# Kernel optimization log

Hardware: AMD Instinct MI355X
Metric: run time of the kernel (lower is better)

The kernel has to match this reference:

```python
import jax, jax.numpy as jnp
import numpy as np

COMMITMENT_COST = 0.25
ENTROPY_WEIGHT = 0.1
EPS = 1e-10


def setup_inputs() -> dict:
    key = jax.random.key(0)
    k1, k2 = jax.random.split(key)
    B, L, D, K = 8, 4096, 256, 4096
    z = jax.random.normal(k1, (B, L, D), dtype=jnp.float32)
    # torch init: uniform(-1/K, 1/K)
    codebook_weight = jax.random.uniform(k2, (K, D), dtype=jnp.float32,
                                         minval=-1.0 / K, maxval=1.0 / K)
    return {"z": z, "codebook_weight": codebook_weight}


def reference(z, codebook_weight):
    B, L, D = z.shape
    z_flat = z.reshape(-1, D)                       # [N, D]
    # squared euclidean distances: [N, K]
    d2 = (jnp.sum(z_flat ** 2, axis=1, keepdims=True)
          + jnp.sum(codebook_weight ** 2, axis=1)
          - 2.0 * z_flat @ codebook_weight.T)
    indices = jnp.argmin(d2, axis=1)                # [N]
    z_q_flat = codebook_weight[indices]             # gather [N, D]
    z_q = z_q_flat.reshape(B, L, D)

    codebook_loss = jnp.mean((z_q - jax.lax.stop_gradient(z)) ** 2)
    commitment_loss = jnp.mean((jax.lax.stop_gradient(z_q) - z) ** 2)

    probs = jax.nn.softmax(-d2, axis=1)             # [N, K]
    avg_probs = probs.mean(axis=0)                  # [K]
    entropy = -jnp.sum(avg_probs * jnp.log(avg_probs + EPS))
    entropy_loss = -entropy

    codebook_commitment_loss = codebook_loss + COMMITMENT_COST * commitment_loss
    scaled_entropy_loss = ENTROPY_WEIGHT * entropy_loss
    vq_loss = codebook_commitment_loss + scaled_entropy_loss

    # straight-through estimator
    z_q_ste = z + jax.lax.stop_gradient(z_q - z)
    indices_out = indices.reshape(B, L)
    return (z_q_ste, indices_out, vq_loss, codebook_commitment_loss, scaled_entropy_loss)
```

## Files before the change

kernel.cpp:

```cpp
#include <hip/hip_runtime.h>
#include <stdint.h>

#define NROWS 32768
#define KC 4096
#define DIM 256
#define BM 32
#define NCT 128
#define TPW 32
#define CAP 40
#define KAPPA 0.99960f
#define K2L2E 2.88539008f
#define L2E 1.44269504f

#define OUT_IDX (NROWS * DIM)
#define OUT_SCAL (OUT_IDX + NROWS)

#define WS_CNORM 0
#define WS_ZNORM 16384
#define WS_LOSS  147456
#define WS_AVGP8 147712
#define WS_FRAG  278784

typedef __bf16 bf8 __attribute__((ext_vector_type(8)));
typedef float f16v __attribute__((ext_vector_type(16)));

__device__ __forceinline__ unsigned ford(float f) {
  unsigned u = __float_as_uint(f);
  return (u & 0x80000000u) ? ~u : (u | 0x80000000u);
}

__device__ __forceinline__ float np_rownorm256(const float* __restrict__ p) {
  float h[2];
  #pragma unroll
  for (int half = 0; half < 2; ++half) {
    const float* b = p + half * 128;
    float r[8];
    #pragma unroll
    for (int j = 0; j < 8; ++j) { float v = b[j]; r[j] = __fmul_rn(v, v); }
    for (int i = 8; i < 128; i += 8) {
      #pragma unroll
      for (int j = 0; j < 8; ++j) {
        float v = b[i + j];
        r[j] = __fadd_rn(r[j], __fmul_rn(v, v));
      }
    }
    h[half] = __fadd_rn(
        __fadd_rn(__fadd_rn(r[0], r[1]), __fadd_rn(r[2], r[3])),
        __fadd_rn(__fadd_rn(r[4], r[5]), __fadd_rn(r[6], r[7])));
  }
  return __fadd_rn(h[0], h[1]);
}

__global__ void k_norms(const float* __restrict__ cbw, const float* __restrict__ z,
                        float* __restrict__ cnorm, float* __restrict__ znorm) {
  int r = blockIdx.x * 256 + threadIdx.x;
  if (r < KC) cnorm[r] = np_rownorm256(cbw + (size_t)r * DIM);
  else {
    int q = r - KC;
    if (q < NROWS) znorm[q] = np_rownorm256(z + (size_t)q * DIM);
  }
}

__global__ void k_frag(const float* __restrict__ cbw, __bf16* __restrict__ frag) {
  int idx = blockIdx.x * 256 + threadIdx.x;
  int c = idx >> 5, u = idx & 31;
  int ds = u >> 1, half = u & 1;
  int ct = c >> 5, m = c & 31;
  int lane = half * 32 + m;
  const float* src = cbw + (size_t)c * DIM + ds * 16 + half * 8;
  float4 a = *(const float4*)src;
  float4 b = *(const float4*)(src + 4);
  bf8 h;
  h[0] = (__bf16)a.x; h[1] = (__bf16)a.y; h[2] = (__bf16)a.z; h[3] = (__bf16)a.w;
  h[4] = (__bf16)b.x; h[5] = (__bf16)b.y; h[6] = (__bf16)b.z; h[7] = (__bf16)b.w;
  *(bf8*)(frag + ((size_t)(ct * 16 + ds) * 64 + lane) * 8) = h;
}

__device__ __forceinline__ float exact_d2(const float* __restrict__ zr,
                                          const float* __restrict__ cr,
                                          float rn, float cn) {
  float mm = 0.f;
  for (int d = 0; d < DIM; d += 4) {
    float4 zv = *(const float4*)(zr + d);
    float4 cv = *(const float4*)(cr + d);
    mm = __builtin_fmaf(zv.x, cv.x, mm);
    mm = __builtin_fmaf(zv.y, cv.y, mm);
    mm = __builtin_fmaf(zv.z, cv.z, mm);
    mm = __builtin_fmaf(zv.w, cv.w, mm);
  }
  return __fsub_rn(__fadd_rn(rn, cn), __fmul_rn(2.f, mm));
}

__device__ __forceinline__ void tile_mfma(const __bf16* __restrict__ Aimg,
                                          const __bf16* __restrict__ tb,
                                          int lane, f16v& acc) {
  #pragma unroll
  for (int r = 0; r < 16; ++r) acc[r] = 0.f;
  #pragma unroll
  for (int ds = 0; ds < 16; ++ds) {
    bf8 Bf = *(const bf8*)(tb + (ds * 64 + lane) * 8);
    bf8 Af = *(const bf8*)&Aimg[((size_t)ds * 64 + lane) * 8];
    acc = __builtin_amdgcn_mfma_f32_32x32x16_bf16(Af, Bf, acc, 0, 0, 0);
  }
}

__global__ __launch_bounds__(256, 4) void k_main(
    const float* __restrict__ z, const float* __restrict__ cbw,
    const float* __restrict__ cnorm, const float* __restrict__ znorm,
    const __bf16* __restrict__ frag, float* __restrict__ out,
    float* __restrict__ avgp8, double* __restrict__ losssum) {
  __shared__ __bf16 Aimg[16 * 64 * 8];
  union CP { int cand[BM][CAP]; float pcol[KC]; };
  __shared__ CP cp;
  __shared__ int ccount[BM];
  __shared__ unsigned rowmaxU[BM];
  __shared__ unsigned long long rowkey[BM];
  __shared__ float esumL[BM], invR[BM], lred[256];
  __shared__ int idxr[BM];

  const int t = threadIdx.x;
  const int lane = t & 63, wv = t >> 6;
  const int ln31 = lane & 31, lh = lane >> 5;
  const int row0 = blockIdx.x * BM;

  if (t < BM) {
    ccount[t] = 0; rowmaxU[t] = 0u; rowkey[t] = ~0ULL; esumL[t] = 0.f;
  }

  #pragma unroll
  for (int i = 0; i < 4; ++i) {
    int idx = t * 4 + i;
    int l = idx & 63, ds = idx >> 6;
    int row = l & 31, d0 = ds * 16 + (l >> 5) * 8;
    const float* src = z + (size_t)(row0 + row) * DIM + d0;
    float4 a = *(const float4*)src;
    float4 b = *(const float4*)(src + 4);
    bf8 h;
    h[0] = (__bf16)a.x; h[1] = (__bf16)a.y; h[2] = (__bf16)a.z; h[3] = (__bf16)a.w;
    h[4] = (__bf16)b.x; h[5] = (__bf16)b.y; h[6] = (__bf16)b.z; h[7] = (__bf16)b.w;
    *(bf8*)&Aimg[((size_t)ds * 64 + l) * 8] = h;
  }
  __syncthreads();

  {
    const int ct = wv * TPW;
    f16v acc;
    tile_mfma(Aimg, frag + (size_t)ct * 8192, lane, acc);
    const float cnl = cnorm[ct * 32 + ln31] * L2E;
    #pragma unroll
    for (int r = 0; r < 16; ++r) {
      const int row = (r & 3) + 8 * (r >> 2) + 4 * lh;
      float e = exp2f(__builtin_fmaf(acc[r], K2L2E, -cnl));
      atomicMax(&rowmaxU[row], __float_as_uint(e));
    }
  }
  __syncthreads();

  float es[16], em[16];
  #pragma unroll
  for (int i = 0; i < 16; ++i) { es[i] = 0.f; em[i] = 0.f; }

  for (int ti = 0; ti < TPW; ++ti) {
    const int ct = wv * TPW + ti;
    f16v acc;
    tile_mfma(Aimg, frag + (size_t)ct * 8192, lane, acc);
    const float cnl = cnorm[ct * 32 + ln31] * L2E;
    #pragma unroll
    for (int r = 0; r < 16; ++r) {
      const int row = (r & 3) + 8 * (r >> 2) + 4 * lh;
      float e = exp2f(__builtin_fmaf(acc[r], K2L2E, -cnl));
      es[r] += e;
      float rm = fmaxf(em[r], __uint_as_float(rowmaxU[row]));
      if (e > rm) { atomicMax(&rowmaxU[row], __float_as_uint(e)); rm = e; }
      em[r] = rm;
      if (e >= rm * KAPPA) {
        int slot = atomicAdd(&ccount[row], 1);
        if (slot < CAP) cp.cand[row][slot] = ct * 32 + ln31;
      }
    }
  }

  #pragma unroll
  for (int r = 0; r < 16; ++r) {
    float e = es[r];
    #pragma unroll
    for (int off = 16; off > 0; off >>= 1) e += __shfl_xor(e, off);
    if (ln31 == 0) {
      const int row = (r & 3) + 8 * (r >> 2) + 4 * lh;
      atomicAdd(&esumL[row], e);
    }
  }
  __syncthreads();
  if (t < BM) invR[t] = 1.0f / esumL[t];
  __syncthreads();

  {
    int r = t & 31, q = t >> 5;
    int cnt = ccount[r];
    const float* zr = z + (size_t)(row0 + r) * DIM;
    float rn = znorm[row0 + r];
    if (cnt <= CAP) {
      for (int s = q; s < cnt; s += 8) {
        int k = cp.cand[r][s];
        float d2 = exact_d2(zr, cbw + (size_t)k * DIM, rn, cnorm[k]);
        atomicMin(&rowkey[r], (((unsigned long long)ford(d2)) << 32) | (unsigned)k);
      }
    } else {
      for (int k = q; k < KC; k += 8) {
        float d2 = exact_d2(zr, cbw + (size_t)k * DIM, rn, cnorm[k]);
        atomicMin(&rowkey[r], (((unsigned long long)ford(d2)) << 32) | (unsigned)k);
      }
    }
  }
  __syncthreads();
  if (t < BM) {
    int idx = (int)(rowkey[t] & 0xFFFFFFFFULL);
    idxr[t] = idx;
    out[OUT_IDX + row0 + t] = (float)idx;
  }
  __syncthreads();

  float lacc = 0.f;
  for (int r = 0; r < BM; ++r) {
    int idx = idxr[r];
    float zq = cbw[(size_t)idx * DIM + t];
    float zv = z[(size_t)(row0 + r) * DIM + t];
    float df = __fsub_rn(zq, zv);
    out[(size_t)(row0 + r) * DIM + t] = __fadd_rn(zv, df);
    lacc += df * df;
  }
  lred[t] = lacc;
  __syncthreads();
  #pragma unroll
  for (int s = 128; s > 0; s >>= 1) {
    if (t < s) lred[t] += lred[t + s];
    __syncthreads();
  }
  if (t == 0) atomicAdd(losssum, (double)lred[0]);

  float ir[16];
  #pragma unroll
  for (int r = 0; r < 16; ++r)
    ir[r] = invR[(r & 3) + 8 * (r >> 2) + 4 * lh];
  __syncthreads();

  for (int ti = 0; ti < TPW; ++ti) {
    const int ct = wv * TPW + ti;
    f16v acc;
    tile_mfma(Aimg, frag + (size_t)ct * 8192, lane, acc);
    const float cnl = cnorm[ct * 32 + ln31] * L2E;
    float s = 0.f;
    #pragma unroll
    for (int r = 0; r < 16; ++r) {
      float e = exp2f(__builtin_fmaf(acc[r], K2L2E, -cnl));
      s = __builtin_fmaf(e, ir[r], s);
    }
    s += __shfl_xor(s, 32);
    if (lh == 0) cp.pcol[ct * 32 + ln31] = s;
  }
  __syncthreads();
  {
    float* shadow = avgp8 + (size_t)(blockIdx.x & 7) * KC;
    #pragma unroll
    for (int i = 0; i < 16; ++i)
      atomicAdd(&shadow[t + 256 * i], cp.pcol[t + 256 * i]);
  }
}

__global__ void k_final(const float* __restrict__ avgp8,
                        const double* __restrict__ losssum,
                        float* __restrict__ out) {
  const int t = threadIdx.x;
  double part = 0.0;
  for (int k = t; k < KC; k += 256) {
    float a4 = 0.f;
    #pragma unroll
    for (int s = 0; s < 8; ++s) a4 += avgp8[s * KC + k];
    double a = (double)a4 / (double)NROWS;
    part += a * log(a + 1e-10);
  }
  __shared__ double sd[256];
  sd[t] = part;
  __syncthreads();
  for (int s = 128; s > 0; s >>= 1) {
    if (t < s) sd[t] += sd[t + s];
    __syncthreads();
  }
  if (t == 0) {
    double H = -sd[0];
    double mse = losssum[0] / (double)((size_t)NROWS * DIM);
    double ccl = 1.25 * mse;
    double sel = -0.1 * H;
    out[OUT_SCAL + 0] = (float)(ccl + sel);
    out[OUT_SCAL + 1] = (float)ccl;
    out[OUT_SCAL + 2] = (float)sel;
  }
}

extern "C" void kernel_launch(void* const* d_in, const int* in_sizes, int n_in,
                              void* d_out, int out_size, void* d_ws, size_t ws_size,
                              hipStream_t stream) {
  const float* z = (const float*)d_in[0];
  const float* cbw = (const float*)d_in[1];
  float* out = (float*)d_out;
  char* ws = (char*)d_ws;
  float* cnorm = (float*)(ws + WS_CNORM);
  float* znorm = (float*)(ws + WS_ZNORM);
  double* losssum = (double*)(ws + WS_LOSS);
  float* avgp8 = (float*)(ws + WS_AVGP8);
  __bf16* frag = (__bf16*)(ws + WS_FRAG);

  hipMemsetAsync(ws + WS_LOSS, 0, 8, stream);
  hipMemsetAsync(ws + WS_AVGP8, 0, 8 * KC * 4, stream);
  k_norms<<<(KC + NROWS) / 256, 256, 0, stream>>>(cbw, z, cnorm, znorm);
  k_frag<<<(KC * 32) / 256, 256, 0, stream>>>(cbw, frag);
  k_main<<<NROWS / BM, 256, 0, stream>>>(z, cbw, cnorm, znorm, frag, out,
                                         avgp8, losssum);
  k_final<<<1, 256, 0, stream>>>(avgp8, losssum, out);
}
```

Before: 477.6 us.

## Register double-buffer codebook fragments and batch candidate atomics in main loops

The codebook B-fragments for the next tile are now prefetched into registers while the current tile's MFMAs issue, replacing per-tile global loads that stalled before each MFMA chain. Row maxima are read once per tile as float4 vectors, and candidate atomics are deferred behind a per-lane bitmask so the common no-candidate path avoids shared atomics. Occupancy is lowered from 4 to 3 blocks per SM to make room for the 64 extra registers of prefetched fragments. The thresholding now uses a slightly staler shared row max, which may admit more candidates but still bounded by CAP.

```diff
diff --git a/kernel.cpp b/kernel.cpp
--- a/kernel.cpp
+++ b/kernel.cpp
@@ -91,20 +91,7 @@
   return __fsub_rn(__fadd_rn(rn, cn), __fmul_rn(2.f, mm));
 }
 
-__device__ __forceinline__ void tile_mfma(const __bf16* __restrict__ Aimg,
-                                          const __bf16* __restrict__ tb,
-                                          int lane, f16v& acc) {
-  #pragma unroll
-  for (int r = 0; r < 16; ++r) acc[r] = 0.f;
-  #pragma unroll
-  for (int ds = 0; ds < 16; ++ds) {
-    bf8 Bf = *(const bf8*)(tb + (ds * 64 + lane) * 8);
-    bf8 Af = *(const bf8*)&Aimg[((size_t)ds * 64 + lane) * 8];
-    acc = __builtin_amdgcn_mfma_f32_32x32x16_bf16(Af, Bf, acc, 0, 0, 0);
-  }
-}
-
-__global__ __launch_bounds__(256, 4) void k_main(
+__global__ __launch_bounds__(256, 3) void k_main(
     const float* __restrict__ z, const float* __restrict__ cbw,
     const float* __restrict__ cnorm, const float* __restrict__ znorm,
     const __bf16* __restrict__ frag, float* __restrict__ out,
@@ -142,11 +129,28 @@
   }
   __syncthreads();
 
-  {
-    const int ct = wv * TPW;
+  const int ctbase = wv * TPW;
+
+  bf8 bq[16];
+  {
+    const __bf16* tb = frag + (size_t)ctbase * 8192;
+    #pragma unroll
+    for (int ds = 0; ds < 16; ++ds)
+      bq[ds] = *(const bf8*)(tb + (ds * 64 + lane) * 8);
+  }
+
+  {
+    const float cnl = cnorm[ctbase * 32 + ln31] * L2E;
+    const __bf16* tb = frag + (size_t)ctbase * 8192;
     f16v acc;
-    tile_mfma(Aimg, frag + (size_t)ct * 8192, lane, acc);
-    const float cnl = cnorm[ct * 32 + ln31] * L2E;
+    #pragma unroll
+    for (int r = 0; r < 16; ++r) acc[r] = 0.f;
+    #pragma unroll
+    for (int ds = 0; ds < 16; ++ds) {
+      bf8 Af = *(const bf8*)&Aimg[((size_t)ds * 64 + lane) * 8];
+      acc = __builtin_amdgcn_mfma_f32_32x32x16_bf16(Af, bq[ds], acc, 0, 0, 0);
+      bq[ds] = *(const bf8*)(tb + (ds * 64 + lane) * 8);
+    }
     #pragma unroll
     for (int r = 0; r < 16; ++r) {
       const int row = (r & 3) + 8 * (r >> 2) + 4 * lh;
@@ -161,21 +165,50 @@
   for (int i = 0; i < 16; ++i) { es[i] = 0.f; em[i] = 0.f; }
 
   for (int ti = 0; ti < TPW; ++ti) {
-    const int ct = wv * TPW + ti;
+    const int ct = ctbase + ti;
+    const int ctn = ctbase + ((ti + 1) & (TPW - 1));
+    const float cnl = cnorm[ct * 32 + ln31] * L2E;
+    const __bf16* tbn = frag + (size_t)ctn * 8192;
+
+    float cr[16];
+    {
+      const float4* rmf = (const float4*)rowmaxU;
+      float4 c0 = rmf[lh], c1 = rmf[2 + lh], c2 = rmf[4 + lh], c3 = rmf[6 + lh];
+      cr[0]=c0.x; cr[1]=c0.y; cr[2]=c0.z; cr[3]=c0.w;
+      cr[4]=c1.x; cr[5]=c1.y; cr[6]=c1.z; cr[7]=c1.w;
+      cr[8]=c2.x; cr[9]=c2.y; cr[10]=c2.z; cr[11]=c2.w;
+      cr[12]=c3.x; cr[13]=c3.y; cr[14]=c3.z; cr[15]=c3.w;
+    }
+
     f16v acc;
-    tile_mfma(Aimg, frag + (size_t)ct * 8192, lane, acc);
-    const float cnl = cnorm[ct * 32 + ln31] * L2E;
+    #pragma unroll
+    for (int r = 0; r < 16; ++r) acc[r] = 0.f;
+    #pragma unroll
+    for (int ds = 0; ds < 16; ++ds) {
+      bf8 Af = *(const bf8*)&Aimg[((size_t)ds * 64 + lane) * 8];
+      acc = __builtin_amdgcn_mfma_f32_32x32x16_bf16(Af, bq[ds], acc, 0, 0, 0);
+      bq[ds] = *(const bf8*)(tbn + (ds * 64 + lane) * 8);
+    }
+
+    unsigned cond = 0u;
     #pragma unroll
     for (int r = 0; r < 16; ++r) {
-      const int row = (r & 3) + 8 * (r >> 2) + 4 * lh;
       float e = exp2f(__builtin_fmaf(acc[r], K2L2E, -cnl));
       es[r] += e;
-      float rm = fmaxf(em[r], __uint_as_float(rowmaxU[row]));
-      if (e > rm) { atomicMax(&rowmaxU[row], __float_as_uint(e)); rm = e; }
-      em[r] = rm;
-      if (e >= rm * KAPPA) {
-        int slot = atomicAdd(&ccount[row], 1);
-        if (slot < CAP) cp.cand[row][slot] = ct * 32 + ln31;
+      float m = fmaxf(em[r], e);
+      em[r] = m;
+      float rm = fmaxf(m, cr[r]);
+      cond |= (e >= rm * KAPPA) ? (1u << r) : 0u;
+    }
+    if (cond) {
+      #pragma unroll
+      for (int r = 0; r < 16; ++r) {
+        if (cond & (1u << r)) {
+          const int row = (r & 3) + 8 * (r >> 2) + 4 * lh;
+          atomicMax(&rowmaxU[row], __float_as_uint(em[r]));
+          int slot = atomicAdd(&ccount[row], 1);
+          if (slot < CAP) cp.cand[row][slot] = ct * 32 + ln31;
+        }
       }
     }
   }
@@ -244,11 +277,26 @@
     ir[r] = invR[(r & 3) + 8 * (r >> 2) + 4 * lh];
   __syncthreads();
 
+  {
+    const __bf16* tb0 = frag + (size_t)ctbase * 8192;
+    #pragma unroll
+    for (int ds = 0; ds < 16; ++ds)
+      bq[ds] = *(const bf8*)(tb0 + (ds * 64 + lane) * 8);
+  }
   for (int ti = 0; ti < TPW; ++ti) {
-    const int ct = wv * TPW + ti;
+    const int ct = ctbase + ti;
+    const int ctn = ctbase + ((ti + 1) & (TPW - 1));
+    const float cnl = cnorm[ct * 32 + ln31] * L2E;
+    const __bf16* tbn = frag + (size_t)ctn * 8192;
     f16v acc;
-    tile_mfma(Aimg, frag + (size_t)ct * 8192, lane, acc);
-    const float cnl = cnorm[ct * 32 + ln31] * L2E;
+    #pragma unroll
+    for (int r = 0; r < 16; ++r) acc[r] = 0.f;
+    #pragma unroll
+    for (int ds = 0; ds < 16; ++ds) {
+      bf8 Af = *(const bf8*)&Aimg[((size_t)ds * 64 + lane) * 8];
+      acc = __builtin_amdgcn_mfma_f32_32x32x16_bf16(Af, bq[ds], acc, 0, 0, 0);
+      bq[ds] = *(const bf8*)(tbn + (ds * 64 + lane) * 8);
+    }
     float s = 0.f;
     #pragma unroll
     for (int r = 0; r < 16; ++r) {
```

After: 849.4 us. 1.78x slower.

## Double block to 512 threads and batch candidate filtering per tile

Applied to the files above, without the earlier changes.

Raises the main kernel to 8 wavefronts per block, so each wave handles 16 codebook tiles instead of 32, and adjusts the staging, refine, output and reduction loops to match. The candidate pass now snapshots the shared row-max values once per tile and builds a bitmask of passing rows. Atomics run only for rows that pass, which removes the per-element shared read and branch from the hot loop. The snapshot can be stale within a tile, so more candidates may pass the KAPPA threshold and overflow CAP, which would trigger the full fallback scan. The larger block may also lower occupancy.

```diff
diff --git a/kernel.cpp b/kernel.cpp
--- a/kernel.cpp
+++ b/kernel.cpp
@@ -6,7 +6,8 @@
 #define DIM 256
 #define BM 32
 #define NCT 128
-#define TPW 32
+#define NWV 8
+#define TPW 16
 #define CAP 40
 #define KAPPA 0.99960f
 #define K2L2E 2.88539008f
@@ -104,7 +105,7 @@
   }
 }
 
-__global__ __launch_bounds__(256, 4) void k_main(
+__global__ __launch_bounds__(512, 4) void k_main(
     const float* __restrict__ z, const float* __restrict__ cbw,
     const float* __restrict__ cnorm, const float* __restrict__ znorm,
     const __bf16* __restrict__ frag, float* __restrict__ out,
@@ -115,7 +116,7 @@
   __shared__ int ccount[BM];
   __shared__ unsigned rowmaxU[BM];
   __shared__ unsigned long long rowkey[BM];
-  __shared__ float esumL[BM], invR[BM], lred[256];
+  __shared__ float esumL[BM], invR[BM], lred[512];
   __shared__ int idxr[BM];
 
   const int t = threadIdx.x;
@@ -128,8 +129,8 @@
   }
 
   #pragma unroll
-  for (int i = 0; i < 4; ++i) {
-    int idx = t * 4 + i;
+  for (int i = 0; i < 2; ++i) {
+    int idx = t * 2 + i;
     int l = idx & 63, ds = idx >> 6;
     int row = l & 31, d0 = ds * 16 + (l >> 5) * 8;
     const float* src = z + (size_t)(row0 + row) * DIM + d0;
@@ -142,11 +143,12 @@
   }
   __syncthreads();
 
+  const int ctbase = wv * TPW;
+
   {
-    const int ct = wv * TPW;
     f16v acc;
-    tile_mfma(Aimg, frag + (size_t)ct * 8192, lane, acc);
-    const float cnl = cnorm[ct * 32 + ln31] * L2E;
+    tile_mfma(Aimg, frag + (size_t)ctbase * 8192, lane, acc);
+    const float cnl = cnorm[ctbase * 32 + ln31] * L2E;
     #pragma unroll
     for (int r = 0; r < 16; ++r) {
       const int row = (r & 3) + 8 * (r >> 2) + 4 * lh;
@@ -156,26 +158,44 @@
   }
   __syncthreads();
 
-  float es[16], em[16];
-  #pragma unroll
-  for (int i = 0; i < 16; ++i) { es[i] = 0.f; em[i] = 0.f; }
+  float es[16];
+  #pragma unroll
+  for (int i = 0; i < 16; ++i) es[i] = 0.f;
 
   for (int ti = 0; ti < TPW; ++ti) {
-    const int ct = wv * TPW + ti;
+    const int ct = ctbase + ti;
+    const float cnl = cnorm[ct * 32 + ln31] * L2E;
+
+    float cr[16];
+    {
+      const float4* rmf = (const float4*)rowmaxU;
+      float4 c0 = rmf[lh], c1 = rmf[2 + lh], c2 = rmf[4 + lh], c3 = rmf[6 + lh];
+      cr[0]  = c0.x; cr[1]  = c0.y; cr[2]  = c0.z; cr[3]  = c0.w;
+      cr[4]  = c1.x; cr[5]  = c1.y; cr[6]  = c1.z; cr[7]  = c1.w;
+      cr[8]  = c2.x; cr[9]  = c2.y; cr[10] = c2.z; cr[11] = c2.w;
+      cr[12] = c3.x; cr[13] = c3.y; cr[14] = c3.z; cr[15] = c3.w;
+    }
+
     f16v acc;
     tile_mfma(Aimg, frag + (size_t)ct * 8192, lane, acc);
-    const float cnl = cnorm[ct * 32 + ln31] * L2E;
+
+    unsigned cond = 0u;
     #pragma unroll
     for (int r = 0; r < 16; ++r) {
-      const int row = (r & 3) + 8 * (r >> 2) + 4 * lh;
       float e = exp2f(__builtin_fmaf(acc[r], K2L2E, -cnl));
       es[r] += e;
-      float rm = fmaxf(em[r], __uint_as_float(rowmaxU[row]));
-      if (e > rm) { atomicMax(&rowmaxU[row], __float_as_uint(e)); rm = e; }
-      em[r] = rm;
-      if (e >= rm * KAPPA) {
-        int slot = atomicAdd(&ccount[row], 1);
-        if (slot < CAP) cp.cand[row][slot] = ct * 32 + ln31;
+      cond |= (e >= cr[r] * KAPPA) ? (1u << r) : 0u;
+    }
+    if (cond) {
+      #pragma unroll
+      for (int r = 0; r < 16; ++r) {
+        if (cond & (1u << r)) {
+          const int row = (r & 3) + 8 * (r >> 2) + 4 * lh;
+          float e = exp2f(__builtin_fmaf(acc[r], K2L2E, -cnl));
+          atomicMax(&rowmaxU[row], __float_as_uint(e));
+          int slot = atomicAdd(&ccount[row], 1);
+          if (slot < CAP) cp.cand[row][slot] = ct * 32 + ln31;
+        }
       }
     }
   }
@@ -200,13 +220,13 @@
     const float* zr = z + (size_t)(row0 + r) * DIM;
     float rn = znorm[row0 + r];
     if (cnt <= CAP) {
-      for (int s = q; s < cnt; s += 8) {
+      for (int s = q; s < cnt; s += 16) {
         int k = cp.cand[r][s];
         float d2 = exact_d2(zr, cbw + (size_t)k * DIM, rn, cnorm[k]);
         atomicMin(&rowkey[r], (((unsigned long long)ford(d2)) << 32) | (unsigned)k);
       }
     } else {
-      for (int k = q; k < KC; k += 8) {
+      for (int k = q; k < KC; k += 16) {
         float d2 = exact_d2(zr, cbw + (size_t)k * DIM, rn, cnorm[k]);
         atomicMin(&rowkey[r], (((unsigned long long)ford(d2)) << 32) | (unsigned)k);
       }
@@ -221,18 +241,21 @@
   __syncthreads();
 
   float lacc = 0.f;
-  for (int r = 0; r < BM; ++r) {
-    int idx = idxr[r];
-    float zq = cbw[(size_t)idx * DIM + t];
-    float zv = z[(size_t)(row0 + r) * DIM + t];
-    float df = __fsub_rn(zq, zv);
-    out[(size_t)(row0 + r) * DIM + t] = __fadd_rn(zv, df);
-    lacc += df * df;
+  {
+    const int col = t & 255;
+    for (int r = (t >> 8); r < BM; r += 2) {
+      int idx = idxr[r];
+      float zq = cbw[(size_t)idx * DIM + col];
+      float zv = z[(size_t)(row0 + r) * DIM + col];
+      float df = __fsub_rn(zq, zv);
+      out[(size_t)(row0 + r) * DIM + col] = __fadd_rn(zv, df);
+      lacc += df * df;
+    }
   }
   lred[t] = lacc;
   __syncthreads();
   #pragma unroll
-  for (int s = 128; s > 0; s >>= 1) {
+  for (int s = 256; s > 0; s >>= 1) {
     if (t < s) lred[t] += lred[t + s];
     __syncthreads();
   }
@@ -245,7 +268,7 @@
   __syncthreads();
 
   for (int ti = 0; ti < TPW; ++ti) {
-    const int ct = wv * TPW + ti;
+    const int ct = ctbase + ti;
     f16v acc;
     tile_mfma(Aimg, frag + (size_t)ct * 8192, lane, acc);
     const float cnl = cnorm[ct * 32 + ln31] * L2E;
@@ -262,8 +285,8 @@
   {
     float* shadow = avgp8 + (size_t)(blockIdx.x & 7) * KC;
     #pragma unroll
-    for (int i = 0; i < 16; ++i)
-      atomicAdd(&shadow[t + 256 * i], cp.pcol[t + 256 * i]);
+    for (int i = 0; i < 8; ++i)
+      atomicAdd(&shadow[t + 512 * i], cp.pcol[t + 512 * i]);
   }
 }
 
@@ -314,7 +337,7 @@
   hipMemsetAsync(ws + WS_AVGP8, 0, 8 * KC * 4, stream);
   k_norms<<<(KC + NROWS) / 256, 256, 0, stream>>>(cbw, z, cnorm, znorm);
   k_frag<<<(KC * 32) / 256, 256, 0, stream>>>(cbw, frag);
-  k_main<<<NROWS / BM, 256, 0, stream>>>(z, cbw, cnorm, znorm, frag, out,
+  k_main<<<NROWS / BM, 512, 0, stream>>>(z, cbw, cnorm, znorm, frag, out,
                                          avgp8, losssum);
   k_final<<<1, 256, 0, stream>>>(avgp8, losssum, out);
 }
```

After: 464.5 us. -2.7%, faster.
